# Kernel tuning notes

Hardware: AMD Instinct MI355X
Metric: run time of the kernel (lower is better)

## Reference

```python
import jax, jax.numpy as jnp
import numpy as np

B, S, E = 4, 2048, 1024
H, DK = 16, 64

def setup_inputs() -> dict:
    key = jax.random.key(0)
    ks = jax.random.split(key, 9)
    sc = 1.0 / np.sqrt(E)
    return {
        "q": jax.random.normal(ks[0], (B, S, E), jnp.float32),
        "Wq": jax.random.normal(ks[1], (E, H * DK), jnp.float32) * sc,
        "bq": jax.random.normal(ks[2], (H * DK,), jnp.float32) * 0.01,
        "Wk": jax.random.normal(ks[3], (E, H * DK), jnp.float32) * sc,
        "bk": jax.random.normal(ks[4], (H * DK,), jnp.float32) * 0.01,
        "Wv": jax.random.normal(ks[5], (E, H * DK), jnp.float32) * sc,
        "bv": jax.random.normal(ks[6], (H * DK,), jnp.float32) * 0.01,
        "Wo": jax.random.normal(ks[7], (H * DK, E), jnp.float32) * sc,
        "bo": jax.random.normal(ks[8], (E,), jnp.float32) * 0.01,
    }

def _split_heads(x):
    # (B, S, H*DK) -> (B, H, S, DK)
    return x.reshape(B, S, H, DK).transpose(0, 2, 1, 3)

def reference(q, Wq, bq, Wk, bk, Wv, bv, Wo, bo):
    # self-attention: k = v = q (torch module path when k=v=None)
    qh = _split_heads(q @ Wq + bq)
    kh = _split_heads(q @ Wk + bk)
    vh = _split_heads(q @ Wv + bv)
    scale = 1.0 / jnp.sqrt(jnp.asarray(DK, qh.dtype))
    scores = jnp.einsum("bhqd,bhkd->bhqk", qh, kh) * scale  # (B,H,S,S)
    attn = jax.nn.softmax(scores, axis=-1)
    ctx = jnp.einsum("bhqk,bhkd->bhqd", attn, vh)
    ctx = ctx.transpose(0, 2, 1, 3).reshape(B, S, H * DK)
    return ctx @ Wo + bo
```

## Files before the change

### kernel.cpp

```cpp
#include <hip/hip_runtime.h>
#include <hip/hip_bf16.h>
#include <math.h>


typedef _Float16 f16x8 __attribute__((ext_vector_type(8)));
typedef _Float16 f16x4 __attribute__((ext_vector_type(4)));
typedef _Float16 f16x2 __attribute__((ext_vector_type(2)));
typedef float    f32x4 __attribute__((ext_vector_type(4)));
typedef unsigned int u32x2 __attribute__((ext_vector_type(2)));
typedef unsigned int u32x4 __attribute__((ext_vector_type(4)));

#define MFMA16(a,b,c) __builtin_amdgcn_mfma_f32_16x16x32_f16(a,b,c,0,0,0)

__device__ __forceinline__ void async_cp16(const _Float16* g, _Float16* l) {
    __builtin_amdgcn_global_load_lds(
        (const __attribute__((address_space(1))) unsigned int*)g,
        (__attribute__((address_space(3))) unsigned int*)l,
        16, 0, 0);
}

__device__ __forceinline__ f16x2 pk(float a, float b) {
    return __builtin_bit_cast(f16x2, __builtin_amdgcn_cvt_pkrtz(a, b));
}

__global__ void __launch_bounds__(256) prep_weights(
    const float* __restrict__ Wq, const float* __restrict__ Wk,
    const float* __restrict__ Wv, const float* __restrict__ Wo,
    _Float16* __restrict__ wt)
{
    __shared__ float tile[32][33];
    int mat = blockIdx.y;
    const float* W = (mat==0)?Wq:(mat==1)?Wk:(mat==2)?Wv:Wo;
    _Float16* WT = wt + (size_t)mat*1048576;
    int t = blockIdx.x;
    int kb = (t & 31) * 32;
    int nb = (t >> 5) * 32;
    int tx = threadIdx.x & 31, ty = threadIdx.x >> 5;
    #pragma unroll
    for (int r = 0; r < 4; ++r) {
        int row = ty + r*8;
        tile[row][tx] = W[(size_t)(kb+row)*1024 + nb + tx];
    }
    __syncthreads();
    #pragma unroll
    for (int r = 0; r < 4; ++r) {
        int row = ty + r*8;
        WT[(size_t)(nb+row)*1024 + kb + tx] = (_Float16)tile[tx][row];
    }
}

__global__ void __launch_bounds__(256) cvt_x(
    const float* __restrict__ X, _Float16* __restrict__ Xh)
{
    int i = (blockIdx.x*256 + threadIdx.x)*4;
    f32x4 x = *(const f32x4*)&X[i];
    f16x4 h;
    #pragma unroll
    for (int k=0;k<4;k++) h[k] = (_Float16)x[k];
    *(f16x4*)&Xh[i] = h;
}

__global__ void __launch_bounds__(256) gemm_qkv(
    const _Float16* __restrict__ Xh, const _Float16* __restrict__ wt,
    const float* __restrict__ bq, const float* __restrict__ bk, const float* __restrict__ bv,
    _Float16* __restrict__ Q, _Float16* __restrict__ K, _Float16* __restrict__ Vt)
{
    __shared__ __align__(16) _Float16 sA[8192];
    __shared__ __align__(16) _Float16 sB[8192];

    const int id = blockIdx.x;
    const int msub = id & 7;
    const int t2 = id >> 3;
    const int nblk = t2 % 24;
    const int mblk = (t2 / 24) * 8 + msub;

    const int tid = threadIdx.x;
    const int wave = tid >> 6, lane = tid & 63;
    const int wr = wave >> 1, wc = wave & 1;
    const int q4 = lane >> 4, cc = lane & 15;

    const int mat = nblk >> 3;
    const int colbase = (nblk & 7) * 128;
    const _Float16* Bg = wt + (size_t)mat*1048576 + (size_t)colbase*1024;
    const _Float16* Ag = Xh + (size_t)mblk*131072;

    f32x4 acc[4][4] = {};

    const int srow = tid >> 3;
    const int scg  = ((tid & 7) ^ ((tid >> 3) & 7)) * 8;

    for (int kb = 0; kb < 1024; kb += 64) {
        __syncthreads();
        #pragma unroll
        for (int rr = 0; rr < 4; ++rr) {
            async_cp16(&Ag[(size_t)(rr*32 + srow)*1024 + kb + scg], sA + rr*2048 + wave*512);
            async_cp16(&Bg[(size_t)(rr*32 + srow)*1024 + kb + scg], sB + rr*2048 + wave*512);
        }
        __syncthreads();
        #pragma unroll
        for (int ks = 0; ks < 2; ++ks) {
            f16x8 af[4], bf[4];
            #pragma unroll
            for (int i=0;i<4;i++){
                af[i] = *(const f16x8*)&sA[(wr*64+i*16+cc)*64 + ((ks*4+q4)^(cc&7))*8];
                bf[i] = *(const f16x8*)&sB[(wc*64+i*16+cc)*64 + ((ks*4+q4)^(cc&7))*8];
            }
            #pragma unroll
            for (int i=0;i<4;i++)
                #pragma unroll
                for (int j=0;j<4;j++)
                    acc[i][j] = MFMA16(af[i], bf[j], acc[i][j]);
        }
    }

    const float* bias = (mat==0)?bq:(mat==1)?bk:bv;
    const float QSCALE = 0.125f * 1.44269504f;
    #pragma unroll
    for (int i=0;i<4;i++)
      #pragma unroll
      for (int j=0;j<4;j++)
        #pragma unroll
        for (int r=0;r<4;r++){
            int m = mblk*128 + wr*64 + i*16 + q4*4 + r;
            int ncol = colbase + wc*64 + j*16 + cc;
            float val = acc[i][j][r] + bias[ncol];
            int b = m >> 11, s = m & 2047;
            int h = ncol >> 6, dk = ncol & 63;
            if (mat == 2) {
                Vt[((size_t)(b*16+h)*64 + dk)*2048 + s] = (_Float16)val;
            } else {
                size_t qi = ((size_t)(b*16+h)*2048 + s)*64 + dk;
                if (mat == 0) Q[qi] = (_Float16)(val * QSCALE);
                else          K[qi] = (_Float16)val;
            }
        }
}

__global__ void __launch_bounds__(256,3) attn(
    const _Float16* __restrict__ Qg, const _Float16* __restrict__ Kg,
    const _Float16* __restrict__ Vg,
    _Float16* __restrict__ Ctx)
{
    __shared__ __align__(16) _Float16 sK[128][72];
    __shared__ __align__(16) _Float16 sV[64][136];

    const int id = blockIdx.x;
    const int xcd = id & 7;
    const int t2 = id >> 3;
    const int qc = t2 & 15;
    const int bh = (t2 >> 4) * 8 + xcd;

    const int tid = threadIdx.x;
    const int wave = tid >> 6, lane = tid & 63;
    const int q4 = lane >> 4, cc = lane & 15;

    const size_t hoff = (size_t)bh * 131072;
    const _Float16* Qp = Qg + hoff;
    const _Float16* Kp = Kg + hoff;
    const _Float16* Vp = Vg + hoff;

    const int qbase = qc*128 + wave*32;

    f16x8 qf[2][2];
    #pragma unroll
    for (int m=0;m<2;m++)
      #pragma unroll
      for (int ks=0;ks<2;ks++)
        qf[m][ks] = *(const f16x8*)&Qp[(qbase+m*16+cc)*64 + ks*32 + q4*8];

    f32x4 o[2][4] = {};
    float lsum[2] = {0.f, 0.f};

    const int r0 = tid >> 3, c8 = (tid & 7)*8;
    const int vrow = tid >> 4, vg = (tid & 15)*8;

    f16x8 kr[4], vr[4];
    #pragma unroll
    for (int p=0;p<4;p++){
        kr[p] = *(const f16x8*)&Kp[(p*32 + r0)*64 + c8];
        vr[p] = *(const f16x8*)&Vp[(size_t)(p*16 + vrow)*2048 + vg];
    }

    for (int kt = 0; kt < 16; ++kt) {
        __syncthreads();
        #pragma unroll
        for (int p=0;p<4;p++){
            *(f16x8*)&sK[p*32+r0][c8] = kr[p];
            *(f16x8*)&sV[p*16+vrow][vg] = vr[p];
        }
        __syncthreads();
        if (kt < 15) {
            #pragma unroll
            for (int p=0;p<4;p++){
                kr[p] = *(const f16x8*)&Kp[((kt+1)*128 + p*32 + r0)*64 + c8];
                vr[p] = *(const f16x8*)&Vp[(size_t)(p*16 + vrow)*2048 + (kt+1)*128 + vg];
            }
        }

        #pragma unroll
        for (int ks=0;ks<4;ks++){
            unsigned Ud[2][2], Wd[2][2];
            #pragma unroll
            for (int aa=0;aa<2;aa++){
                int kj = ks*2 + aa;
                f16x8 k0 = *(const f16x8*)&sK[kj*16+cc][q4*8];
                f16x8 k1 = *(const f16x8*)&sK[kj*16+cc][32+q4*8];
                #pragma unroll
                for (int m=0;m<2;m++){
                    f32x4 z = {};
                    f32x4 s = MFMA16(k0, qf[m][0], z);
                    s = MFMA16(k1, qf[m][1], s);
                    float p0 = __builtin_amdgcn_exp2f(s[0]);
                    float p1 = __builtin_amdgcn_exp2f(s[1]);
                    float p2 = __builtin_amdgcn_exp2f(s[2]);
                    float p3 = __builtin_amdgcn_exp2f(s[3]);
                    lsum[m] += (p0 + p1) + (p2 + p3);
                    unsigned d0 = __builtin_bit_cast(unsigned, pk(p0, p1));
                    unsigned d1 = __builtin_bit_cast(unsigned, pk(p2, p3));
                    if (aa == 0) { Ud[m][0] = d0; Ud[m][1] = d1; }
                    else         { Wd[m][0] = d0; Wd[m][1] = d1; }
                }
            }
            f16x8 pa[2];
            #pragma unroll
            for (int m=0;m<2;m++){
                u32x2 x0 = __builtin_amdgcn_permlane32_swap(Ud[m][0], Wd[m][0], false, false);
                u32x2 r02 = __builtin_amdgcn_permlane16_swap(x0[0], x0[1], false, false);
                u32x2 x1 = __builtin_amdgcn_permlane32_swap(Ud[m][1], Wd[m][1], false, false);
                u32x2 r13 = __builtin_amdgcn_permlane16_swap(x1[0], x1[1], false, false);
                u32x4 pw;
                pw[0] = r02[0]; pw[1] = r13[0]; pw[2] = r02[1]; pw[3] = r13[1];
                pa[m] = __builtin_bit_cast(f16x8, pw);
            }
            #pragma unroll
            for (int v=0;v<4;v++){
                f16x8 vf = *(const f16x8*)&sV[v*16+cc][ks*32+q4*8];
                o[0][v] = MFMA16(pa[0], vf, o[0][v]);
                o[1][v] = MFMA16(pa[1], vf, o[1][v]);
            }
        }
    }

    #pragma unroll
    for (int m=0;m<2;m++){
        lsum[m] += __shfl_xor(lsum[m], 16, 64);
        lsum[m] += __shfl_xor(lsum[m], 32, 64);
    }
    __syncthreads();
    float* sL = (float*)&sK[0][0];
    if (q4 == 0) {
        sL[wave*32 + cc]      = lsum[0];
        sL[wave*32 + 16 + cc] = lsum[1];
    }
    __syncthreads();

    int b = bh >> 4, h = bh & 15;
    #pragma unroll
    for (int m=0;m<2;m++)
      #pragma unroll
      for (int r=0;r<4;r++){
        float inv = 1.f / sL[wave*32 + m*16 + q4*4 + r];
        int s = qbase + m*16 + q4*4 + r;
        #pragma unroll
        for (int v=0;v<4;v++){
            float val = o[m][v][r]*inv;
            int dk = v*16 + cc;
            Ctx[((size_t)(b*2048+s)*16 + h)*64 + dk] = (_Float16)val;
        }
      }
}

__global__ void __launch_bounds__(256) gemm_out(
    const _Float16* __restrict__ Ctx, const _Float16* __restrict__ wt,
    const float* __restrict__ bo,
    float* __restrict__ out)
{
    __shared__ __align__(16) _Float16 sA[8192];
    __shared__ __align__(16) _Float16 sB[8192];

    const int id = blockIdx.x;
    const int msub = id & 7;
    const int t2 = id >> 3;
    const int nblk = t2 & 7;
    const int mblk = (t2 >> 3) * 8 + msub;

    const int tid = threadIdx.x;
    const int wave = tid >> 6, lane = tid & 63;
    const int wr = wave >> 1, wc = wave & 1;
    const int q4 = lane >> 4, cc = lane & 15;

    const _Float16* Bg = wt + (size_t)3*1048576 + (size_t)nblk*128*1024;
    const _Float16* Ag = Ctx + (size_t)mblk*131072;

    f32x4 acc[4][4] = {};
    const int srow = tid >> 3;
    const int scg  = ((tid & 7) ^ ((tid >> 3) & 7)) * 8;

    for (int kb = 0; kb < 1024; kb += 64) {
        __syncthreads();
        #pragma unroll
        for (int rr = 0; rr < 4; ++rr) {
            async_cp16(&Ag[(size_t)(rr*32 + srow)*1024 + kb + scg], sA + rr*2048 + wave*512);
            async_cp16(&Bg[(size_t)(rr*32 + srow)*1024 + kb + scg], sB + rr*2048 + wave*512);
        }
        __syncthreads();
        #pragma unroll
        for (int ks = 0; ks < 2; ++ks) {
            f16x8 af[4], bf[4];
            #pragma unroll
            for (int i=0;i<4;i++){
                af[i] = *(const f16x8*)&sA[(wr*64+i*16+cc)*64 + ((ks*4+q4)^(cc&7))*8];
                bf[i] = *(const f16x8*)&sB[(wc*64+i*16+cc)*64 + ((ks*4+q4)^(cc&7))*8];
            }
            #pragma unroll
            for (int i=0;i<4;i++)
                #pragma unroll
                for (int j=0;j<4;j++)
                    acc[i][j] = MFMA16(af[i], bf[j], acc[i][j]);
        }
    }

    #pragma unroll
    for (int i=0;i<4;i++)
      #pragma unroll
      for (int j=0;j<4;j++)
        #pragma unroll
        for (int r=0;r<4;r++){
            int m = mblk*128 + wr*64 + i*16 + q4*4 + r;
            int n = nblk*128 + wc*64 + j*16 + cc;
            out[(size_t)m*1024 + n] = acc[i][j][r] + bo[n];
        }
}

extern "C" void kernel_launch(void* const* d_in, const int* in_sizes, int n_in,
                              void* d_out, int out_size, void* d_ws, size_t ws_size,
                              hipStream_t stream)
{
    const float* q  = (const float*)d_in[0];
    const float* Wq = (const float*)d_in[1];
    const float* bq = (const float*)d_in[2];
    const float* Wk = (const float*)d_in[3];
    const float* bk = (const float*)d_in[4];
    const float* Wv = (const float*)d_in[5];
    const float* bv = (const float*)d_in[6];
    const float* Wo = (const float*)d_in[7];
    const float* bo = (const float*)d_in[8];
    float* out = (float*)d_out;

    _Float16* ws  = (_Float16*)d_ws;
    _Float16* wt  = ws;
    _Float16* Xh  = ws + 4194304;
    _Float16* Q   = ws + 12582912;
    _Float16* K   = ws + 20971520;
    _Float16* Vt  = ws + 29360128;
    _Float16* Ctx = Xh;

    prep_weights<<<dim3(1024,4), 256, 0, stream>>>(Wq, Wk, Wv, Wo, wt);
    cvt_x<<<dim3(8192), 256, 0, stream>>>(q, Xh);
    gemm_qkv<<<dim3(1536), 256, 0, stream>>>(Xh, wt, bq, bk, bv, Q, K, Vt);
    attn<<<dim3(1024), 256, 0, stream>>>(Q, K, Vt, Ctx);
    gemm_out<<<dim3(512), 256, 0, stream>>>(Ctx, wt, bo, out);
}
```

Before: 303.1 us.

## Triple-buffer GEMM K-loop with async prefetch and enlarge tiles to 256x128

Both projection GEMMs now run a shared K-loop that stages tiles two steps ahead into a three-deep LDS ring. It uses vmcnt-based waits and a single barrier per step instead of two full syncs, so global loads overlap MFMA work. Blocks grow to 512 threads with 256x128 output tiles, which halves the grid and raises A-tile reuse per block. The LDS footprint rises to about 147KB, so only one block fits per CU and occupancy-based latency hiding drops.

Result: no change. 303.8 us (+0.2%).

```diff
diff --git a/kernel.cpp b/kernel.cpp
--- a/kernel.cpp
+++ b/kernel.cpp
@@ -60,13 +60,69 @@
     *(f16x4*)&Xh[i] = h;
 }
 
-__global__ void __launch_bounds__(256) gemm_qkv(
+__device__ __forceinline__ void stage_tile(
+    const _Float16* __restrict__ Ag, const _Float16* __restrict__ Bg, int kb,
+    _Float16* sAb, _Float16* sBb, int wave, int lane)
+{
+    #pragma unroll
+    for (int j = 0; j < 4; ++j) {
+        int d   = j*512 + wave*64 + lane;
+        int row = d >> 3;
+        int sg  = (d & 7) ^ (row & 7);
+        async_cp16(&Ag[(size_t)row*1024 + kb + sg*8], sAb + (j*512 + wave*64)*8);
+    }
+    #pragma unroll
+    for (int j = 0; j < 2; ++j) {
+        int d   = j*512 + wave*64 + lane;
+        int row = d >> 3;
+        int sg  = (d & 7) ^ (row & 7);
+        async_cp16(&Bg[(size_t)row*1024 + kb + sg*8], sBb + (j*512 + wave*64)*8);
+    }
+}
+
+#define GEMM_K_LOOP(EXTRA_STAGE_GUARD)                                         \
+    stage_tile(Ag, Bg, 0,  pA0, pB0, wave, lane);                              \
+    stage_tile(Ag, Bg, 64, pA1, pB1, wave, lane);                              \
+    asm volatile("s_waitcnt vmcnt(6)" ::: "memory");                           \
+    __builtin_amdgcn_s_barrier();                                              \
+    __builtin_amdgcn_sched_barrier(0);                                         \
+    for (int t = 0; t < 16; ++t) {                                             \
+        if (t + 2 < 16) stage_tile(Ag, Bg, (t+2)*64, pA2, pB2, wave, lane);    \
+        f16x8 af[4][2], bf[4][2];                                              \
+        _Pragma("unroll")                                                      \
+        for (int i = 0; i < 4; ++i) {                                          \
+            _Pragma("unroll")                                                  \
+            for (int ks = 0; ks < 2; ++ks) {                                   \
+                af[i][ks] = *(const f16x8*)&pA0[(wr*64+i*16+cc)*64 +           \
+                                                (((ks*4+q4)^(cc&7))*8)];       \
+                bf[i][ks] = *(const f16x8*)&pB0[(wc*64+i*16+cc)*64 +           \
+                                                (((ks*4+q4)^(cc&7))*8)];       \
+            }                                                                  \
+        }                                                                      \
+        __builtin_amdgcn_s_setprio(1);                                         \
+        _Pragma("unroll")                                                      \
+        for (int ks = 0; ks < 2; ++ks)                                         \
+            _Pragma("unroll")                                                  \
+            for (int i = 0; i < 4; ++i)                                        \
+                _Pragma("unroll")                                              \
+                for (int j = 0; j < 4; ++j)                                    \
+                    acc[i][j] = MFMA16(af[i][ks], bf[j][ks], acc[i][j]);       \
+        __builtin_amdgcn_s_setprio(0);                                         \
+        if (t < 14) asm volatile("s_waitcnt vmcnt(6)" ::: "memory");           \
+        else        asm volatile("s_waitcnt vmcnt(0)" ::: "memory");           \
+        __builtin_amdgcn_s_barrier();                                          \
+        __builtin_amdgcn_sched_barrier(0);                                     \
+        _Float16* tA = pA0; pA0 = pA1; pA1 = pA2; pA2 = tA;                    \
+        _Float16* tB = pB0; pB0 = pB1; pB1 = pB2; pB2 = tB;                    \
+    }
+
+__global__ void __launch_bounds__(512) gemm_qkv(
     const _Float16* __restrict__ Xh, const _Float16* __restrict__ wt,
     const float* __restrict__ bq, const float* __restrict__ bk, const float* __restrict__ bv,
     _Float16* __restrict__ Q, _Float16* __restrict__ K, _Float16* __restrict__ Vt)
 {
-    __shared__ __align__(16) _Float16 sA[8192];
-    __shared__ __align__(16) _Float16 sB[8192];
+    __shared__ __align__(16) _Float16 sA[3][16384];
+    __shared__ __align__(16) _Float16 sB[3][8192];
 
     const int id = blockIdx.x;
     const int msub = id & 7;
@@ -82,36 +138,14 @@
     const int mat = nblk >> 3;
     const int colbase = (nblk & 7) * 128;
     const _Float16* Bg = wt + (size_t)mat*1048576 + (size_t)colbase*1024;
-    const _Float16* Ag = Xh + (size_t)mblk*131072;
+    const _Float16* Ag = Xh + (size_t)mblk*262144;
+
+    _Float16 *pA0 = &sA[0][0], *pA1 = &sA[1][0], *pA2 = &sA[2][0];
+    _Float16 *pB0 = &sB[0][0], *pB1 = &sB[1][0], *pB2 = &sB[2][0];
 
     f32x4 acc[4][4] = {};
 
-    const int srow = tid >> 3;
-    const int scg  = ((tid & 7) ^ ((tid >> 3) & 7)) * 8;
-
-    for (int kb = 0; kb < 1024; kb += 64) {
-        __syncthreads();
-        #pragma unroll
-        for (int rr = 0; rr < 4; ++rr) {
-            async_cp16(&Ag[(size_t)(rr*32 + srow)*1024 + kb + scg], sA + rr*2048 + wave*512);
-            async_cp16(&Bg[(size_t)(rr*32 + srow)*1024 + kb + scg], sB + rr*2048 + wave*512);
-        }
-        __syncthreads();
-        #pragma unroll
-        for (int ks = 0; ks < 2; ++ks) {
-            f16x8 af[4], bf[4];
-            #pragma unroll
-            for (int i=0;i<4;i++){
-                af[i] = *(const f16x8*)&sA[(wr*64+i*16+cc)*64 + ((ks*4+q4)^(cc&7))*8];
-                bf[i] = *(const f16x8*)&sB[(wc*64+i*16+cc)*64 + ((ks*4+q4)^(cc&7))*8];
-            }
-            #pragma unroll
-            for (int i=0;i<4;i++)
-                #pragma unroll
-                for (int j=0;j<4;j++)
-                    acc[i][j] = MFMA16(af[i], bf[j], acc[i][j]);
-        }
-    }
+    GEMM_K_LOOP()
 
     const float* bias = (mat==0)?bq:(mat==1)?bk:bv;
     const float QSCALE = 0.125f * 1.44269504f;
@@ -121,7 +155,7 @@
       for (int j=0;j<4;j++)
         #pragma unroll
         for (int r=0;r<4;r++){
-            int m = mblk*128 + wr*64 + i*16 + q4*4 + r;
+            int m = mblk*256 + wr*64 + i*16 + q4*4 + r;
             int ncol = colbase + wc*64 + j*16 + cc;
             float val = acc[i][j][r] + bias[ncol];
             int b = m >> 11, s = m & 2047;
@@ -133,6 +167,47 @@
                 if (mat == 0) Q[qi] = (_Float16)(val * QSCALE);
                 else          K[qi] = (_Float16)val;
             }
+        }
+}
+
+__global__ void __launch_bounds__(512) gemm_out(
+    const _Float16* __restrict__ Ctx, const _Float16* __restrict__ wt,
+    const float* __restrict__ bo,
+    float* __restrict__ out)
+{
+    __shared__ __align__(16) _Float16 sA[3][16384];
+    __shared__ __align__(16) _Float16 sB[3][8192];
+
+    const int id = blockIdx.x;
+    const int msub = id & 7;
+    const int t2 = id >> 3;
+    const int nblk = t2 & 7;
+    const int mblk = (t2 >> 3) * 8 + msub;
+
+    const int tid = threadIdx.x;
+    const int wave = tid >> 6, lane = tid & 63;
+    const int wr = wave >> 1, wc = wave & 1;
+    const int q4 = lane >> 4, cc = lane & 15;
+
+    const _Float16* Bg = wt + (size_t)3*1048576 + (size_t)nblk*128*1024;
+    const _Float16* Ag = Ctx + (size_t)mblk*262144;
+
+    _Float16 *pA0 = &sA[0][0], *pA1 = &sA[1][0], *pA2 = &sA[2][0];
+    _Float16 *pB0 = &sB[0][0], *pB1 = &sB[1][0], *pB2 = &sB[2][0];
+
+    f32x4 acc[4][4] = {};
+
+    GEMM_K_LOOP()
+
+    #pragma unroll
+    for (int i=0;i<4;i++)
+      #pragma unroll
+      for (int j=0;j<4;j++)
+        #pragma unroll
+        for (int r=0;r<4;r++){
+            int m = mblk*256 + wr*64 + i*16 + q4*4 + r;
+            int n = nblk*128 + wc*64 + j*16 + cc;
+            out[(size_t)m*1024 + n] = acc[i][j][r] + bo[n];
         }
 }
 
@@ -270,68 +345,6 @@
       }
 }
 
-__global__ void __launch_bounds__(256) gemm_out(
-    const _Float16* __restrict__ Ctx, const _Float16* __restrict__ wt,
-    const float* __restrict__ bo,
-    float* __restrict__ out)
-{
-    __shared__ __align__(16) _Float16 sA[8192];
-    __shared__ __align__(16) _Float16 sB[8192];
-
-    const int id = blockIdx.x;
-    const int msub = id & 7;
-    const int t2 = id >> 3;
-    const int nblk = t2 & 7;
-    const int mblk = (t2 >> 3) * 8 + msub;
-
-    const int tid = threadIdx.x;
-    const int wave = tid >> 6, lane = tid & 63;
-    const int wr = wave >> 1, wc = wave & 1;
-    const int q4 = lane >> 4, cc = lane & 15;
-
-    const _Float16* Bg = wt + (size_t)3*1048576 + (size_t)nblk*128*1024;
-    const _Float16* Ag = Ctx + (size_t)mblk*131072;
-
-    f32x4 acc[4][4] = {};
-    const int srow = tid >> 3;
-    const int scg  = ((tid & 7) ^ ((tid >> 3) & 7)) * 8;
-
-    for (int kb = 0; kb < 1024; kb += 64) {
-        __syncthreads();
-        #pragma unroll
-        for (int rr = 0; rr < 4; ++rr) {
-            async_cp16(&Ag[(size_t)(rr*32 + srow)*1024 + kb + scg], sA + rr*2048 + wave*512);
-            async_cp16(&Bg[(size_t)(rr*32 + srow)*1024 + kb + scg], sB + rr*2048 + wave*512);
-        }
-        __syncthreads();
-        #pragma unroll
-        for (int ks = 0; ks < 2; ++ks) {
-            f16x8 af[4], bf[4];
-            #pragma unroll
-            for (int i=0;i<4;i++){
-                af[i] = *(const f16x8*)&sA[(wr*64+i*16+cc)*64 + ((ks*4+q4)^(cc&7))*8];
-                bf[i] = *(const f16x8*)&sB[(wc*64+i*16+cc)*64 + ((ks*4+q4)^(cc&7))*8];
-            }
-            #pragma unroll
-            for (int i=0;i<4;i++)
-                #pragma unroll
-                for (int j=0;j<4;j++)
-                    acc[i][j] = MFMA16(af[i], bf[j], acc[i][j]);
-        }
-    }
-
-    #pragma unroll
-    for (int i=0;i<4;i++)
-      #pragma unroll
-      for (int j=0;j<4;j++)
-        #pragma unroll
-        for (int r=0;r<4;r++){
-            int m = mblk*128 + wr*64 + i*16 + q4*4 + r;
-            int n = nblk*128 + wc*64 + j*16 + cc;
-            out[(size_t)m*1024 + n] = acc[i][j][r] + bo[n];
-        }
-}
-
 extern "C" void kernel_launch(void* const* d_in, const int* in_sizes, int n_in,
                               void* d_out, int out_size, void* d_ws, size_t ws_size,
                               hipStream_t stream)
@@ -357,7 +370,7 @@
 
     prep_weights<<<dim3(1024,4), 256, 0, stream>>>(Wq, Wk, Wv, Wo, wt);
     cvt_x<<<dim3(8192), 256, 0, stream>>>(q, Xh);
-    gemm_qkv<<<dim3(1536), 256, 0, stream>>>(Xh, wt, bq, bk, bv, Q, K, Vt);
+    gemm_qkv<<<dim3(768), 512, 0, stream>>>(Xh, wt, bq, bk, bv, Q, K, Vt);
     attn<<<dim3(1024), 256, 0, stream>>>(Q, K, Vt, Ctx);
-    gemm_out<<<dim3(512), 256, 0, stream>>>(Ctx, wt, bo, out);
-}
+    gemm_out<<<dim3(256), 512, 0, stream>>>(Ctx, wt, bo, out);
+}
```
